# Kernel optimization log

Measured on AMD Instinct MI355X. Metric: run time of the kernel, lower is better.

The kernel has to match this reference:

```python
import jax, jax.numpy as jnp
import numpy as np

D_MODEL = 128


def setup_inputs() -> dict:
    key = jax.random.key(0)
    ks = jax.random.split(key, 7)
    d = D_MODEL
    B, N = 4, 512
    # Kaiming-ish init scales for linear layers
    W1 = jax.random.normal(ks[0], (2 * d, d), jnp.float32) / np.sqrt(2 * d)
    b1 = jnp.zeros((d,), jnp.float32)
    W2 = jax.random.normal(ks[1], (d, d // 2), jnp.float32) / np.sqrt(d)
    b2 = jnp.zeros((d // 2,), jnp.float32)
    W3 = jax.random.normal(ks[2], (d // 2, 1), jnp.float32) / np.sqrt(d // 2)
    b3 = jnp.zeros((1,), jnp.float32)
    node_features = jax.random.normal(ks[3], (B, N, d), jnp.float32)
    return {"node_features": node_features, "W1": W1, "b1": b1,
            "W2": W2, "b2": b2, "W3": W3, "b3": b3}


def reference(node_features, W1, b1, W2, b2, W3, b3):
    # node_features: [B, N, d]. Pairwise concat [x_i, x_j] @ W1 is split as
    # x_i @ W1[:d] + x_j @ W1[d:] — same math as cat+Linear, but avoids
    # materializing the [B, N, N, 2d] concat tensor.
    d = node_features.shape[-1]
    hi = jnp.einsum('bnd,dk->bnk', node_features, W1[:d])   # [B, N, d]
    hj = jnp.einsum('bnd,dk->bnk', node_features, W1[d:])   # [B, N, d]
    h = jax.nn.relu(hi[:, :, None, :] + hj[:, None, :, :] + b1)  # [B, N, N, d]
    h = jax.nn.relu(jnp.einsum('bijk,km->bijm', h, W2) + b2)      # [B, N, N, d/2]
    logits = jnp.einsum('bijm,mo->bijo', h, W3) + b3              # [B, N, N, 1]
    return jax.nn.sigmoid(logits[..., 0])                          # [B, N, N]
```

## Files before the change

### kernel.cpp

```cpp
#include <hip/hip_runtime.h>
#include <hip/hip_fp16.h>

#define D_MODEL 128
#define NB 4
#define NN 512

typedef _Float16 f16;
typedef _Float16 f16x8 __attribute__((ext_vector_type(8)));
typedef float f32x4 __attribute__((ext_vector_type(4)));

__global__ __launch_bounds__(256) void prep_kernel(
    const float* __restrict__ x,
    const float* __restrict__ W1,
    const float* __restrict__ b1,
    const float* __restrict__ W2,
    f16* __restrict__ Hi, f16* __restrict__ Hj, f16* __restrict__ W2p)
{
    const int blk = blockIdx.x;
    const int t = threadIdx.x;
    if (blk < 128) {
        const int r0 = blk * 16;
        __shared__ float xs[16][128];
        for (int idx = t; idx < 16 * 128; idx += 256)
            xs[idx >> 7][idx & 127] = x[(size_t)r0 * 128 + idx];
        __syncthreads();

        const int isJ = t >> 7;
        const int k = t & 127;
        const float* wcol = W1 + (isJ ? 128 * 128 : 0) + k;
        float acc[16];
        #pragma unroll
        for (int r = 0; r < 16; r++) acc[r] = 0.f;
        for (int d = 0; d < 128; d++) {
            float w = wcol[d * 128];
            #pragma unroll
            for (int r = 0; r < 16; r++) acc[r] = fmaf(xs[r][d], w, acc[r]);
        }
        const float bb = isJ ? 0.f : b1[k];
        f16* dst = isJ ? Hj : Hi;
        #pragma unroll
        for (int r = 0; r < 16; r++)
            dst[(size_t)(r0 + r) * 128 + k] = (f16)(acc[r] + bb);
    } else {
        for (int slot = t; slot < 16 * 64; slot += 256) {
            const int lane = slot & 63;
            const int fidx = slot >> 6;
            const int kt = fidx >> 2, nt = fidx & 3;
            const int krow = kt * 32 + 8 * (lane >> 4);
            const int col = nt * 16 + (lane & 15);
            #pragma unroll
            for (int j = 0; j < 8; j++)
                W2p[(size_t)slot * 8 + j] = (f16)W2[(krow + j) * 64 + col];
        }
    }
}

__global__ __launch_bounds__(256) void pair_kernel(
    const f16* __restrict__ Hi, const f16* __restrict__ Hj,
    const f16* __restrict__ W2p,
    const float* __restrict__ b2, const float* __restrict__ W3,
    const float* __restrict__ b3p, float* __restrict__ out)
{
    const int lane = threadIdx.x & 63;
    const int wave = threadIdx.x >> 6;
    const int bid = blockIdx.x;
    const int jg4 = bid & 7;
    const int ic  = (bid >> 3) & 15;
    const int b   = bid >> 7;
    const int j0 = (jg4 * 4 + wave) * 16;
    const int i0 = ic * 32;

    const int lrow = lane & 15;
    const int lgrp = lane >> 4;

    f16x8 w2f[4][4];
    #pragma unroll
    for (int kt = 0; kt < 4; kt++)
        #pragma unroll
        for (int nt = 0; nt < 4; nt++)
            w2f[kt][nt] = *(const f16x8*)(W2p + (size_t)((kt * 4 + nt) * 64 + lane) * 8);

    const f16* hjbase = Hj + (size_t)(b * NN + j0 + lrow) * 128 + 8 * lgrp;
    f16x8 hjf[4];
    #pragma unroll
    for (int kt = 0; kt < 4; kt++)
        hjf[kt] = *(const f16x8*)(hjbase + kt * 32);

    float b2v[4], w3v[4];
    #pragma unroll
    for (int nt = 0; nt < 4; nt++) {
        b2v[nt] = b2[nt * 16 + lrow];
        w3v[nt] = W3[nt * 16 + lrow];
    }
    const float b3 = b3p[0];

    const f16* hibase = Hi + (size_t)(b * NN + i0) * 128 + 8 * lgrp;
    float* obase = out + ((size_t)b * NN + i0) * NN + j0;

    const f16x8 zero8 = (f16x8)(f16)0;

    #pragma unroll 2
    for (int ii = 0; ii < 32; ii++) {
        f16x8 hif[4];
        #pragma unroll
        for (int kt = 0; kt < 4; kt++)
            hif[kt] = *(const f16x8*)(hibase + ii * 128 + kt * 32);

        f32x4 accD[4];
        #pragma unroll
        for (int nt = 0; nt < 4; nt++) accD[nt] = (f32x4)(0.0f);

        #pragma unroll
        for (int kt = 0; kt < 4; kt++) {
            f16x8 s = hif[kt] + hjf[kt];
            s = __builtin_elementwise_max(s, zero8);
            #pragma unroll
            for (int nt = 0; nt < 4; nt++)
                accD[nt] = __builtin_amdgcn_mfma_f32_16x16x32_f16(s, w2f[kt][nt], accD[nt], 0, 0, 0);
        }

        float acc[4] = {0.f, 0.f, 0.f, 0.f};
        #pragma unroll
        for (int nt = 0; nt < 4; nt++) {
            #pragma unroll
            for (int r = 0; r < 4; r++) {
                float h = fmaxf(accD[nt][r] + b2v[nt], 0.f);
                acc[r] = fmaf(h, w3v[nt], acc[r]);
            }
        }
        #pragma unroll
        for (int r = 0; r < 4; r++) {
            #pragma unroll
            for (int m = 1; m < 16; m <<= 1)
                acc[r] += __shfl_xor(acc[r], m, 64);
        }
        if (lrow == 0) {
            float4 o;
            float lg0 = acc[0] + b3, lg1 = acc[1] + b3, lg2 = acc[2] + b3, lg3 = acc[3] + b3;
            o.x = 1.f / (1.f + __expf(-lg0));
            o.y = 1.f / (1.f + __expf(-lg1));
            o.z = 1.f / (1.f + __expf(-lg2));
            o.w = 1.f / (1.f + __expf(-lg3));
            *(float4*)(obase + (size_t)ii * NN + lgrp * 4) = o;
        }
    }
}

extern "C" void kernel_launch(void* const* d_in, const int* in_sizes, int n_in,
                              void* d_out, int out_size, void* d_ws, size_t ws_size,
                              hipStream_t stream) {
    const float* x  = (const float*)d_in[0];
    const float* W1 = (const float*)d_in[1];
    const float* b1 = (const float*)d_in[2];
    const float* W2 = (const float*)d_in[3];
    const float* b2 = (const float*)d_in[4];
    const float* W3 = (const float*)d_in[5];
    const float* b3 = (const float*)d_in[6];
    float* out = (float*)d_out;

    f16* Hi  = (f16*)d_ws;
    f16* Hj  = Hi + (size_t)NB * NN * 128;
    f16* W2p = Hj + (size_t)NB * NN * 128;

    prep_kernel<<<129, 256, 0, stream>>>(x, W1, b1, W2, Hi, Hj, W2p);
    pair_kernel<<<512, 256, 0, stream>>>(Hi, Hj, W2p, b2, W3, b3, out);
}
```

Baseline: 114.4 us.

## Swap MFMA operands to cut epilogue shuffles and double grid parallelism

Swaps the A/B operands of the MFMA so that each lane's four accumulator rows hold hidden units for a single output pair. The W3 dot product then reduces mostly within the lane and needs only two cross-lane shuffles instead of sixteen. Sigmoid uses a hardware reciprocal and is computed once per lane rather than four times. The prep and pair grids are doubled by halving rows per block, and launch bounds request 4 blocks per CU for more parallelism. The trade-offs are scalar (non-vectorized) output stores and more repeated per-block loads of W2 fragments.

```diff
diff --git a/kernel.cpp b/kernel.cpp
--- a/kernel.cpp
+++ b/kernel.cpp
@@ -18,28 +18,28 @@
 {
     const int blk = blockIdx.x;
     const int t = threadIdx.x;
-    if (blk < 128) {
-        const int r0 = blk * 16;
-        __shared__ float xs[16][128];
-        for (int idx = t; idx < 16 * 128; idx += 256)
+    if (blk < 256) {
+        const int r0 = blk * 8;
+        __shared__ float xs[8][128];
+        for (int idx = t; idx < 8 * 128; idx += 256)
             xs[idx >> 7][idx & 127] = x[(size_t)r0 * 128 + idx];
         __syncthreads();
 
         const int isJ = t >> 7;
         const int k = t & 127;
         const float* wcol = W1 + (isJ ? 128 * 128 : 0) + k;
-        float acc[16];
+        float acc[8];
         #pragma unroll
-        for (int r = 0; r < 16; r++) acc[r] = 0.f;
+        for (int r = 0; r < 8; r++) acc[r] = 0.f;
         for (int d = 0; d < 128; d++) {
             float w = wcol[d * 128];
             #pragma unroll
-            for (int r = 0; r < 16; r++) acc[r] = fmaf(xs[r][d], w, acc[r]);
+            for (int r = 0; r < 8; r++) acc[r] = fmaf(xs[r][d], w, acc[r]);
         }
         const float bb = isJ ? 0.f : b1[k];
         f16* dst = isJ ? Hj : Hi;
         #pragma unroll
-        for (int r = 0; r < 16; r++)
+        for (int r = 0; r < 8; r++)
             dst[(size_t)(r0 + r) * 128 + k] = (f16)(acc[r] + bb);
     } else {
         for (int slot = t; slot < 16 * 64; slot += 256) {
@@ -55,7 +55,7 @@
     }
 }
 
-__global__ __launch_bounds__(256) void pair_kernel(
+__global__ __launch_bounds__(256, 4) void pair_kernel(
     const f16* __restrict__ Hi, const f16* __restrict__ Hj,
     const f16* __restrict__ W2p,
     const float* __restrict__ b2, const float* __restrict__ W3,
@@ -65,10 +65,10 @@
     const int wave = threadIdx.x >> 6;
     const int bid = blockIdx.x;
     const int jg4 = bid & 7;
-    const int ic  = (bid >> 3) & 15;
-    const int b   = bid >> 7;
+    const int ic  = (bid >> 3) & 31;
+    const int b   = bid >> 8;
     const int j0 = (jg4 * 4 + wave) * 16;
-    const int i0 = ic * 32;
+    const int i0 = ic * 16;
 
     const int lrow = lane & 15;
     const int lgrp = lane >> 4;
@@ -86,21 +86,21 @@
     for (int kt = 0; kt < 4; kt++)
         hjf[kt] = *(const f16x8*)(hjbase + kt * 32);
 
-    float b2v[4], w3v[4];
+    f32x4 b2v[4], w3v[4];
     #pragma unroll
     for (int nt = 0; nt < 4; nt++) {
-        b2v[nt] = b2[nt * 16 + lrow];
-        w3v[nt] = W3[nt * 16 + lrow];
+        b2v[nt] = *(const f32x4*)(b2 + nt * 16 + 4 * lgrp);
+        w3v[nt] = *(const f32x4*)(W3 + nt * 16 + 4 * lgrp);
     }
     const float b3 = b3p[0];
 
     const f16* hibase = Hi + (size_t)(b * NN + i0) * 128 + 8 * lgrp;
-    float* obase = out + ((size_t)b * NN + i0) * NN + j0;
+    float* orow = out + ((size_t)b * NN + i0) * NN + j0 + lrow;
 
     const f16x8 zero8 = (f16x8)(f16)0;
 
     #pragma unroll 2
-    for (int ii = 0; ii < 32; ii++) {
+    for (int ii = 0; ii < 16; ii++) {
         f16x8 hif[4];
         #pragma unroll
         for (int kt = 0; kt < 4; kt++)
@@ -116,33 +116,23 @@
             s = __builtin_elementwise_max(s, zero8);
             #pragma unroll
             for (int nt = 0; nt < 4; nt++)
-                accD[nt] = __builtin_amdgcn_mfma_f32_16x16x32_f16(s, w2f[kt][nt], accD[nt], 0, 0, 0);
+                accD[nt] = __builtin_amdgcn_mfma_f32_16x16x32_f16(w2f[kt][nt], s, accD[nt], 0, 0, 0);
         }
 
-        float acc[4] = {0.f, 0.f, 0.f, 0.f};
+        float acc = 0.f;
         #pragma unroll
         for (int nt = 0; nt < 4; nt++) {
             #pragma unroll
             for (int r = 0; r < 4; r++) {
-                float h = fmaxf(accD[nt][r] + b2v[nt], 0.f);
-                acc[r] = fmaf(h, w3v[nt], acc[r]);
+                float h = fmaxf(accD[nt][r] + b2v[nt][r], 0.f);
+                acc = fmaf(h, w3v[nt][r], acc);
             }
         }
-        #pragma unroll
-        for (int r = 0; r < 4; r++) {
-            #pragma unroll
-            for (int m = 1; m < 16; m <<= 1)
-                acc[r] += __shfl_xor(acc[r], m, 64);
-        }
-        if (lrow == 0) {
-            float4 o;
-            float lg0 = acc[0] + b3, lg1 = acc[1] + b3, lg2 = acc[2] + b3, lg3 = acc[3] + b3;
-            o.x = 1.f / (1.f + __expf(-lg0));
-            o.y = 1.f / (1.f + __expf(-lg1));
-            o.z = 1.f / (1.f + __expf(-lg2));
-            o.w = 1.f / (1.f + __expf(-lg3));
-            *(float4*)(obase + (size_t)ii * NN + lgrp * 4) = o;
-        }
+        acc += __shfl_xor(acc, 16, 64);
+        acc += __shfl_xor(acc, 32, 64);
+        float sg = __builtin_amdgcn_rcpf(1.f + __expf(-(acc + b3)));
+        if (lgrp == 0)
+            orow[(size_t)ii * NN] = sg;
     }
 }
 
@@ -162,6 +152,6 @@
     f16* Hj  = Hi + (size_t)NB * NN * 128;
     f16* W2p = Hj + (size_t)NB * NN * 128;
 
-    prep_kernel<<<129, 256, 0, stream>>>(x, W1, b1, W2, Hi, Hj, W2p);
-    pair_kernel<<<512, 256, 0, stream>>>(Hi, Hj, W2p, b2, W3, b3, out);
+    prep_kernel<<<257, 256, 0, stream>>>(x, W1, b1, W2, Hi, Hj, W2p);
+    pair_kernel<<<1024, 256, 0, stream>>>(Hi, Hj, W2p, b2, W3, b3, out);
 }
```

New measurement: 123.0 us. 7.5% more time.
